# Kernel optimization log

Measured on AMD Instinct MI355X. Metric: run time of the kernel, lower is better.

The kernel has to match this reference:

```python
import jax, jax.numpy as jnp
import numpy as np

B_, C, N, M, DX = 4, 8, 1024, 1024, 1
POINTS_PER_UNIT = 64


def setup_inputs() -> dict:
    key = jax.random.key(0)
    k1, k2, k3 = jax.random.split(key, 3)
    xz = jax.random.uniform(k1, (M, DX), dtype=jnp.float32)          # grid locations
    z = jax.random.normal(k2, (B_, C, M, M), dtype=jnp.float32)      # grid encoding
    x = jax.random.normal(k3, (B_, N, DX), dtype=jnp.float32)        # target locations
    log_scale = jnp.log(jnp.float32(2.0 / POINTS_PER_UNIT))          # learned scalar
    return {"xz": xz, "z": z, "x": x, "log_scale": log_scale}


def reference(xz, z, x, log_scale):
    # pairwise squared distances: (b, n, m)
    dists2 = jnp.sum((x[:, :, None, :] - xz[None, None, :, :]) ** 2, axis=-1)
    # RBF weights
    weights = jnp.exp(-0.5 * dists2 / jnp.exp(2.0 * log_scale))      # (b, n, m)
    # weighted interpolation of grid encoding: (b, c, n, m)
    z1 = jnp.einsum("bnm,bcmk->bcnk", weights, z)
    # outer product z1 @ z1^T: (b, c, n, n)
    z2 = jnp.einsum("bcnk,bcok->bcno", z1, z1)
    return (xz, z2)
```

## Files before the change

### kernel.cpp

```cpp
#include <hip/hip_runtime.h>
#include <hip/hip_bf16.h>


typedef __attribute__((ext_vector_type(8))) unsigned short u16x8;
typedef __attribute__((ext_vector_type(8))) __bf16 bf16x8;
typedef __attribute__((ext_vector_type(4))) float f32x4;

typedef __attribute__((address_space(1))) void gvoid;
typedef __attribute__((address_space(3))) void svoid;
#define GLDS(g, s) __builtin_amdgcn_global_load_lds((gvoid*)(g), (svoid*)(s), 16, 0, 0)

__device__ __forceinline__ unsigned short f2bf(float f) {
  unsigned int u = __builtin_bit_cast(unsigned int, f);
  u += 0x7fffu + ((u >> 16) & 1u);
  return (unsigned short)(u >> 16);
}

__device__ __forceinline__ bf16x8 as_bf16x8(u16x8 v) {
  return __builtin_bit_cast(bf16x8, v);
}

__global__ void weights_kernel(const float* __restrict__ xz, const float* __restrict__ x,
                               const float* __restrict__ ls, unsigned short* __restrict__ W) {
  int bn = blockIdx.x;
  float xv = x[bn];
  float coef = -0.5f * __expf(-2.0f * ls[0]);
  unsigned short* Wrow = W + (size_t)bn * 1024;
  #pragma unroll
  for (int i = 0; i < 4; ++i) {
    int m = threadIdx.x + i * 256;
    float d = xv - xz[m];
    Wrow[m] = f2bf(__expf(coef * d * d));
  }
}

__global__ void transpose_kernel(const float* __restrict__ Z, unsigned short* __restrict__ Zt) {
  __shared__ float tile[64][65];
  int bc = blockIdx.z;
  const float* Zp = Z + ((size_t)bc << 20);
  unsigned short* Ztp = Zt + ((size_t)bc << 20);
  int m0 = blockIdx.x * 64, k0 = blockIdx.y * 64;
  int tx = threadIdx.x & 63, tg = threadIdx.x >> 6;
  #pragma unroll
  for (int i = 0; i < 16; ++i) {
    int ml = tg + i * 4;
    tile[ml][tx] = Zp[(size_t)(m0 + ml) * 1024 + k0 + tx];
  }
  __syncthreads();
  int tx2 = (threadIdx.x & 31) * 2, kg = threadIdx.x >> 5;
  #pragma unroll
  for (int i = 0; i < 8; ++i) {
    int kl = kg + i * 8;
    ushort2 v;
    v.x = f2bf(tile[tx2][kl]);
    v.y = f2bf(tile[tx2 + 1][kl]);
    *(ushort2*)&Ztp[(size_t)(k0 + kl) * 1024 + m0 + tx2] = v;
  }
}

template<int TPB, bool OUT_BF16, bool A_PER_B, bool SYMM>
__global__ __launch_bounds__(256) void gemm_nt(const unsigned short* __restrict__ A,
                                               const unsigned short* __restrict__ B,
                                               unsigned short* __restrict__ Cbf,
                                               float* __restrict__ Cf) {
  __shared__ __align__(16) char smem[49152];

  const int chunk = (TPB * 32) >> 3;
  int w = ((int)blockIdx.x & 7) * chunk + ((int)blockIdx.x >> 3);
  int bc = w / TPB;
  int t  = w % TPB;
  int bi, bj;
  if (SYMM) {
    bi = 0;
    while (t >= 8 - bi) { t -= 8 - bi; ++bi; }
    bj = bi + t;
  } else {
    bj = t >> 3; bi = t & 7;
  }

  const unsigned short* Ap = A + ((size_t)(A_PER_B ? (bc >> 3) : bc) << 20);
  const unsigned short* Bp = B + ((size_t)bc << 20);
  const int tid = threadIdx.x;
  const int wave = tid >> 6, lane = tid & 63;
  const int wr = wave >> 1, wc = wave & 1;
  const int la = lane & 15, ha = lane >> 4;
  f32x4 acc[4][4] = {};

  const int c8 = (tid & 3) * 8;
  const unsigned short* gA0 = Ap + (size_t)(bi * 128 + (tid >> 2)) * 1024 + c8;
  const unsigned short* gA1 = gA0 + (size_t)64 * 1024;
  const unsigned short* gB0 = Bp + (size_t)(bj * 128 + (tid >> 2)) * 1024 + c8;
  const unsigned short* gB1 = gB0 + (size_t)64 * 1024;

  auto stage = [&](int slot, int kt) {
    unsigned short* dA = (unsigned short*)(smem + slot * 8192) + wave * 512;
    unsigned short* dB = (unsigned short*)(smem + 24576 + slot * 8192) + wave * 512;
    GLDS(gA0 + kt, dA); GLDS(gA1 + kt, dA + 2048);
    GLDS(gB0 + kt, dB); GLDS(gB1 + kt, dB + 2048);
  };

  stage(0, 0);
  stage(1, 32);
  asm volatile("s_waitcnt vmcnt(4)" ::: "memory");
  __builtin_amdgcn_s_barrier();

  int sl0 = 0, sl1 = 1, sl2 = 2;
  for (int t2 = 0; t2 < 32; ++t2) {
    if (t2 < 30) stage(sl2, (t2 + 2) * 32);
    const unsigned short* rA = (const unsigned short*)(smem + sl0 * 8192);
    const unsigned short* rB = (const unsigned short*)(smem + 24576 + sl0 * 8192);
    u16x8 af[4], bfr[4];
    #pragma unroll
    for (int m = 0; m < 4; ++m)
      af[m] = *(const u16x8*)&rA[(wr * 64 + m * 16 + la) * 32 + ha * 8];
    #pragma unroll
    for (int n = 0; n < 4; ++n)
      bfr[n] = *(const u16x8*)&rB[(wc * 64 + n * 16 + la) * 32 + ha * 8];
    #pragma unroll
    for (int m = 0; m < 4; ++m)
      #pragma unroll
      for (int n = 0; n < 4; ++n)
        acc[m][n] = __builtin_amdgcn_mfma_f32_16x16x32_bf16(
            as_bf16x8(af[m]), as_bf16x8(bfr[n]), acc[m][n], 0, 0, 0);
    if (t2 < 30)       asm volatile("s_waitcnt vmcnt(4)" ::: "memory");
    else if (t2 == 30) asm volatile("s_waitcnt vmcnt(0)" ::: "memory");
    if (t2 < 31) __builtin_amdgcn_s_barrier();
    int tmp = sl0; sl0 = sl1; sl1 = sl2; sl2 = tmp;
  }
  __builtin_amdgcn_s_barrier();

  const size_t cb20 = (size_t)bc << 20;

  if (OUT_BF16) {
    unsigned short* sE = (unsigned short*)smem + wave * 1024;
    #pragma unroll
    for (int m = 0; m < 4; ++m) {
      #pragma unroll
      for (int n = 0; n < 4; ++n)
        #pragma unroll
        for (int j = 0; j < 4; ++j)
          sE[(ha * 4 + j) * 64 + n * 16 + la] = f2bf(acc[m][n][j]);
      int rrow = lane >> 2;
      int cch  = (lane & 3) * 16;
      u16x8 v0 = *(const u16x8*)&sE[rrow * 64 + cch];
      u16x8 v1 = *(const u16x8*)&sE[rrow * 64 + cch + 8];
      unsigned short* gp = Cbf + cb20 +
          (size_t)(bi * 128 + wr * 64 + m * 16 + rrow) * 1024 + bj * 128 + wc * 64 + cch;
      *(u16x8*)gp = v0;
      *(u16x8*)(gp + 8) = v1;
      __builtin_amdgcn_s_barrier();
    }
  } else {
    #pragma unroll
    for (int m = 0; m < 4; ++m) {
      int row0 = bi * 128 + wr * 64 + m * 16 + ha * 4;
      #pragma unroll
      for (int n = 0; n < 4; ++n) {
        int col = bj * 128 + wc * 64 + n * 16 + la;
        #pragma unroll
        for (int j = 0; j < 4; ++j)
          Cf[cb20 + (size_t)(row0 + j) * 1024 + col] = acc[m][n][j];
      }
    }
    if (SYMM && bi != bj) {
      float (*sT)[129] = (float(*)[129])smem;
      #pragma unroll
      for (int b = 0; b < 4; ++b) {
        if (wr == (b >> 1)) {
          #pragma unroll
          for (int dm = 0; dm < 2; ++dm) {
            int m = (b & 1) * 2 + dm;
            #pragma unroll
            for (int n = 0; n < 4; ++n)
              #pragma unroll
              for (int j = 0; j < 4; ++j)
                sT[dm * 16 + ha * 4 + j][wc * 64 + n * 16 + la] = acc[m][n][j];
          }
        }
        __syncthreads();
        int c  = tid >> 1;
        int r0 = (tid & 1) * 16;
        float* gp = Cf + cb20 + (size_t)(bj * 128 + c) * 1024 + bi * 128 + b * 32 + r0;
        #pragma unroll
        for (int q = 0; q < 4; ++q) {
          f32x4 v;
          #pragma unroll
          for (int k = 0; k < 4; ++k) v[k] = sT[r0 + q * 4 + k][c];
          *(f32x4*)(gp + q * 4) = v;
        }
        __syncthreads();
      }
    }
  }
}

extern "C" void kernel_launch(void* const* d_in, const int* in_sizes, int n_in,
                              void* d_out, int out_size, void* d_ws, size_t ws_size,
                              hipStream_t stream) {
  const float* xz = (const float*)d_in[0];
  const float* z  = (const float*)d_in[1];
  const float* x  = (const float*)d_in[2];
  const float* ls = (const float*)d_in[3];
  float* out = (float*)d_out;

  unsigned short* W  = (unsigned short*)d_ws;
  unsigned short* Zt = W + ((size_t)4 << 20);
  unsigned short* z1 = Zt + ((size_t)32 << 20);

  hipMemcpyAsync(out, xz, 1024 * sizeof(float), hipMemcpyDeviceToDevice, stream);
  weights_kernel<<<4096, 256, 0, stream>>>(xz, x, ls, W);
  transpose_kernel<<<dim3(16, 16, 32), 256, 0, stream>>>(z, Zt);
  gemm_nt<64, true,  true,  false><<<32 * 64, 256, 0, stream>>>(W,  Zt, z1, nullptr);
  gemm_nt<36, false, false, true ><<<32 * 36, 256, 0, stream>>>(z1, z1, nullptr, out + 1024);
}
```

Measured before the change: 187.0 us.

## Swizzle LDS tile layout and use double-buffering for the symmetric GEMM

Changes how global_load_lds writes A/B tiles into shared memory by using an XOR-swizzled row/chunk mapping, so the 16-byte fragment reads for MFMA avoid LDS bank conflicts. Adds a STAGES template parameter: the first GEMM keeps the 3-stage pipeline, while the second (symmetric, fp32 output) GEMM uses a 2-stage double buffer with less LDS and a higher occupancy hint in launch_bounds. The double-buffered path waits on vmcnt(0) every iteration, which exposes more load latency in exchange for more resident blocks.

```diff
diff --git a/kernel.cpp b/kernel.cpp
--- a/kernel.cpp
+++ b/kernel.cpp
@@ -58,12 +58,13 @@
   }
 }
 
-template<int TPB, bool OUT_BF16, bool A_PER_B, bool SYMM>
-__global__ __launch_bounds__(256) void gemm_nt(const unsigned short* __restrict__ A,
-                                               const unsigned short* __restrict__ B,
-                                               unsigned short* __restrict__ Cbf,
-                                               float* __restrict__ Cf) {
-  __shared__ __align__(16) char smem[49152];
+template<int STAGES, int TPB, bool OUT_BF16, bool A_PER_B, bool SYMM>
+__global__ __launch_bounds__(256, (STAGES == 3) ? 3 : 5)
+void gemm_nt(const unsigned short* __restrict__ A,
+             const unsigned short* __restrict__ B,
+             unsigned short* __restrict__ Cbf,
+             float* __restrict__ Cf) {
+  __shared__ __align__(16) char smem[STAGES * 16384];
 
   const int chunk = (TPB * 32) >> 3;
   int w = ((int)blockIdx.x & 7) * chunk + ((int)blockIdx.x >> 3);
@@ -86,46 +87,69 @@
   const int la = lane & 15, ha = lane >> 4;
   f32x4 acc[4][4] = {};
 
-  const int c8 = (tid & 3) * 8;
-  const unsigned short* gA0 = Ap + (size_t)(bi * 128 + (tid >> 2)) * 1024 + c8;
-  const unsigned short* gA1 = gA0 + (size_t)64 * 1024;
-  const unsigned short* gB0 = Bp + (size_t)(bj * 128 + (tid >> 2)) * 1024 + c8;
-  const unsigned short* gB1 = gB0 + (size_t)64 * 1024;
+  const int slog = (lane & 7) ^ ((lane >> 3) & 7);
+  const int rloc = 2 * (lane >> 3) + (slog & 1);
+  const int cloc = (slog >> 1) * 8;
+  const unsigned short* gA0 = Ap + (size_t)(bi * 128 + (wave * 2)     * 16 + rloc) * 1024 + cloc;
+  const unsigned short* gA1 = Ap + (size_t)(bi * 128 + (wave * 2 + 1) * 16 + rloc) * 1024 + cloc;
+  const unsigned short* gB0 = Bp + (size_t)(bj * 128 + (wave * 2)     * 16 + rloc) * 1024 + cloc;
+  const unsigned short* gB1 = Bp + (size_t)(bj * 128 + (wave * 2 + 1) * 16 + rloc) * 1024 + cloc;
 
   auto stage = [&](int slot, int kt) {
-    unsigned short* dA = (unsigned short*)(smem + slot * 8192) + wave * 512;
-    unsigned short* dB = (unsigned short*)(smem + 24576 + slot * 8192) + wave * 512;
-    GLDS(gA0 + kt, dA); GLDS(gA1 + kt, dA + 2048);
-    GLDS(gB0 + kt, dB); GLDS(gB1 + kt, dB + 2048);
+    char* dA = smem + slot * 8192 + wave * 2048;
+    char* dB = smem + STAGES * 8192 + slot * 8192 + wave * 2048;
+    GLDS(gA0 + kt, dA); GLDS(gA1 + kt, dA + 1024);
+    GLDS(gB0 + kt, dB); GLDS(gB1 + kt, dB + 1024);
   };
 
-  stage(0, 0);
-  stage(1, 32);
-  asm volatile("s_waitcnt vmcnt(4)" ::: "memory");
-  __builtin_amdgcn_s_barrier();
-
-  int sl0 = 0, sl1 = 1, sl2 = 2;
-  for (int t2 = 0; t2 < 32; ++t2) {
-    if (t2 < 30) stage(sl2, (t2 + 2) * 32);
-    const unsigned short* rA = (const unsigned short*)(smem + sl0 * 8192);
-    const unsigned short* rB = (const unsigned short*)(smem + 24576 + sl0 * 8192);
+  const int sphys = ((ha << 1) | (la & 1)) ^ (la >> 1);
+  const int aoff = wr * 4096 + (la >> 1) * 128 + sphys * 16;
+  const int boff = wc * 4096 + (la >> 1) * 128 + sphys * 16;
+
+  auto compute = [&](int slot) {
+    const char* rA = smem + slot * 8192;
+    const char* rB = smem + STAGES * 8192 + slot * 8192;
     u16x8 af[4], bfr[4];
     #pragma unroll
-    for (int m = 0; m < 4; ++m)
-      af[m] = *(const u16x8*)&rA[(wr * 64 + m * 16 + la) * 32 + ha * 8];
-    #pragma unroll
-    for (int n = 0; n < 4; ++n)
-      bfr[n] = *(const u16x8*)&rB[(wc * 64 + n * 16 + la) * 32 + ha * 8];
+    for (int m = 0; m < 4; ++m) af[m]  = *(const u16x8*)(rA + aoff + m * 1024);
+    #pragma unroll
+    for (int n = 0; n < 4; ++n) bfr[n] = *(const u16x8*)(rB + boff + n * 1024);
     #pragma unroll
     for (int m = 0; m < 4; ++m)
       #pragma unroll
       for (int n = 0; n < 4; ++n)
         acc[m][n] = __builtin_amdgcn_mfma_f32_16x16x32_bf16(
             as_bf16x8(af[m]), as_bf16x8(bfr[n]), acc[m][n], 0, 0, 0);
-    if (t2 < 30)       asm volatile("s_waitcnt vmcnt(4)" ::: "memory");
-    else if (t2 == 30) asm volatile("s_waitcnt vmcnt(0)" ::: "memory");
-    if (t2 < 31) __builtin_amdgcn_s_barrier();
-    int tmp = sl0; sl0 = sl1; sl1 = sl2; sl2 = tmp;
+  };
+
+  if constexpr (STAGES == 3) {
+    stage(0, 0);
+    stage(1, 32);
+    asm volatile("s_waitcnt vmcnt(4)" ::: "memory");
+    __builtin_amdgcn_s_barrier();
+    int sl0 = 0, sl1 = 1, sl2 = 2;
+    for (int t2 = 0; t2 < 32; ++t2) {
+      if (t2 < 30) stage(sl2, (t2 + 2) * 32);
+      compute(sl0);
+      if (t2 < 30)       asm volatile("s_waitcnt vmcnt(4)" ::: "memory");
+      else if (t2 == 30) asm volatile("s_waitcnt vmcnt(0)" ::: "memory");
+      if (t2 < 31) __builtin_amdgcn_s_barrier();
+      int tmp = sl0; sl0 = sl1; sl1 = sl2; sl2 = tmp;
+    }
+  } else {
+    stage(0, 0);
+    asm volatile("s_waitcnt vmcnt(0)" ::: "memory");
+    __builtin_amdgcn_s_barrier();
+    int cur = 0;
+    for (int t2 = 0; t2 < 32; ++t2) {
+      if (t2 < 31) stage(cur ^ 1, (t2 + 1) * 32);
+      compute(cur);
+      if (t2 < 31) {
+        asm volatile("s_waitcnt vmcnt(0)" ::: "memory");
+        __builtin_amdgcn_s_barrier();
+      }
+      cur ^= 1;
+    }
   }
   __builtin_amdgcn_s_barrier();
 
@@ -210,6 +234,6 @@
   hipMemcpyAsync(out, xz, 1024 * sizeof(float), hipMemcpyDeviceToDevice, stream);
   weights_kernel<<<4096, 256, 0, stream>>>(xz, x, ls, W);
   transpose_kernel<<<dim3(16, 16, 32), 256, 0, stream>>>(z, Zt);
-  gemm_nt<64, true,  true,  false><<<32 * 64, 256, 0, stream>>>(W,  Zt, z1, nullptr);
-  gemm_nt<36, false, false, true ><<<32 * 36, 256, 0, stream>>>(z1, z1, nullptr, out + 1024);
-}
+  gemm_nt<3, 64, true,  true,  false><<<32 * 64, 256, 0, stream>>>(W,  Zt, z1, nullptr);
+  gemm_nt<2, 36, false, false, true ><<<32 * 36, 256, 0, stream>>>(z1, z1, nullptr, out + 1024);
+}
```

Result: slower. 202.8 us (+8.4%).
